# Kernel tuning notes

Hardware: AMD Instinct MI355X
Metric: run time of the kernel (lower is better)

The kernel has to match this reference:

```python
import jax, jax.numpy as jnp
import numpy as np

N_NODES = 100000
N_EDGES = 1600000
F_IN = 16
H = 64
N_LAYERS = 2
LN_EPS = 1e-5


def setup_inputs() -> dict:
    key = jax.random.key(0)
    ks = jax.random.split(key, 12)
    x = jax.random.normal(ks[0], (N_NODES, F_IN), dtype=jnp.float32)
    edge_index = jax.random.randint(ks[1], (2, N_EDGES), 0, N_NODES, dtype=jnp.int64)
    s = lambda fan_in: 1.0 / np.sqrt(fan_in)
    Wp = jax.random.uniform(ks[2], (H, F_IN), jnp.float32, -s(F_IN), s(F_IN))
    bp = jax.random.uniform(ks[3], (H,), jnp.float32, -s(F_IN), s(F_IN))
    # Per-layer SAGEConv params: lin_l (neighbor agg, with bias) and lin_r (root, no bias)
    Wl = jax.random.uniform(ks[4], (N_LAYERS, H, H), jnp.float32, -s(H), s(H))
    bl = jax.random.uniform(ks[5], (N_LAYERS, H), jnp.float32, -s(H), s(H))
    Wr = jax.random.uniform(ks[6], (N_LAYERS, H, H), jnp.float32, -s(H), s(H))
    gamma = jnp.ones((N_LAYERS, H), jnp.float32)
    beta = jnp.zeros((N_LAYERS, H), jnp.float32)
    W1 = jax.random.uniform(ks[7], (H // 2, H), jnp.float32, -s(H), s(H))
    b1 = jax.random.uniform(ks[8], (H // 2,), jnp.float32, -s(H), s(H))
    W2 = jax.random.uniform(ks[9], (1, H // 2), jnp.float32, -s(H // 2), s(H // 2))
    b2 = jax.random.uniform(ks[10], (1,), jnp.float32, -s(H // 2), s(H // 2))
    return {"x": x, "edge_index": edge_index, "Wp": Wp, "bp": bp, "Wl": Wl,
            "bl": bl, "Wr": Wr, "gamma": gamma, "beta": beta,
            "W1": W1, "b1": b1, "W2": W2, "b2": b2}


def _layernorm(h, g, b):
    mu = jnp.mean(h, axis=-1, keepdims=True)
    var = jnp.mean(jnp.square(h - mu), axis=-1, keepdims=True)
    return (h - mu) * jax.lax.rsqrt(var + LN_EPS) * g + b


def reference(x, edge_index, Wp, bp, Wl, bl, Wr, gamma, beta, W1, b1, W2, b2):
    N = x.shape[0]
    src, dst = edge_index[0], edge_index[1]
    # input projection + relu
    h = jax.nn.relu(x @ Wp.T + bp)  # [N, H]
    # in-degree for mean aggregation (empty-neighborhood mean -> 0, so clamp is safe
    # only because random graph; matches scatter_mean semantics via masked divide)
    deg = jax.ops.segment_sum(jnp.ones(src.shape, jnp.float32), dst, num_segments=N)
    inv_deg = jnp.where(deg > 0, 1.0 / jnp.maximum(deg, 1.0), 0.0)[:, None]  # [N,1]
    for i in range(Wl.shape[0]):
        identity = h
        agg = jax.ops.segment_sum(h[src], dst, num_segments=N) * inv_deg  # mean over neighbors
        out = agg @ Wl[i].T + bl[i] + h @ Wr[i].T  # SAGEConv
        out = _layernorm(out, gamma[i], beta[i])
        h = jax.nn.relu(out) + identity  # dropout inactive at eval
    h = jax.nn.relu(h @ W1.T + b1)
    y = h @ W2.T + b2  # [N, 1]
    return y.squeeze(-1)
```

## Files before the change

### kernel.cpp

```cpp
#include <hip/hip_runtime.h>
#include <hip/hip_fp16.h>

#define FIN 16
#define HH 64
#define BKT_SHIFT 9
#define BSZ (1 << BKT_SHIFT)
#define MAXBUCK 256
#define NBLK 128

static constexpr float LN_EPS = 1e-5f;

__device__ __forceinline__ float laneval(float v, int l) {
  return __uint_as_float(__builtin_amdgcn_readlane(__float_as_uint(v), l));
}
__device__ __forceinline__ int rfl(int v) { return __builtin_amdgcn_readfirstlane(v); }
__device__ __forceinline__ float rflf(float v) {
  return __uint_as_float(__builtin_amdgcn_readfirstlane(__float_as_uint(v)));
}

__global__ void k_detect(const unsigned int* ei, int E, int* flag) {
  int lane = threadIdx.x & 63;
  int n = (E < 64) ? E : 64;
  unsigned int hi = (lane < n) ? ei[2 * lane + 1] : 0u;
  unsigned long long nz = __ballot(hi != 0u);
  if (lane == 0) *flag = (nz == 0ull) ? 1 : 0;
}


__global__ __launch_bounds__(256) void k_bincount(const void* ei, int E,
                                                  const int* __restrict__ flag,
                                                  int* __restrict__ Cmat, int nbuck) {
  __shared__ int lh[MAXBUCK];
  const int is64 = *flag;
  int t = threadIdx.x, j = blockIdx.x;
  for (int b = t; b < nbuck; b += 256) lh[b] = 0;
  __syncthreads();
  int chunk = (E + gridDim.x - 1) / gridDim.x;
  int e0 = j * chunk, e1 = (e0 + chunk < E) ? (e0 + chunk) : E;
  for (int e = e0 + t; e < e1; e += 256) {
    int d = is64 ? (int)((const long long*)ei)[E + e] : ((const int*)ei)[E + e];
    atomicAdd(&lh[d >> BKT_SHIFT], 1);
  }
  __syncthreads();
  for (int b = t; b < nbuck; b += 256) Cmat[b * gridDim.x + j] = lh[b];
}

__global__ void k_scanC(int* __restrict__ C, int len) {
  __shared__ int sm[1024];
  __shared__ int carry;
  int t = threadIdx.x;
  if (t == 0) carry = 0;
  __syncthreads();
  for (int base = 0; base < len; base += 1024) {
    int i = base + t;
    int v = (i < len) ? C[i] : 0;
    sm[t] = v;
    __syncthreads();
    for (int off = 1; off < 1024; off <<= 1) {
      int x = (t >= off) ? sm[t - off] : 0;
      __syncthreads();
      sm[t] += x;
      __syncthreads();
    }
    if (i < len) C[i] = carry + sm[t] - v;
    __syncthreads();
    if (t == 0) carry += sm[1023];
    __syncthreads();
  }
}

__global__ __launch_bounds__(256) void k_binwrite(const void* ei, int E,
                                                  const int* __restrict__ flag,
                                                  const int* __restrict__ Cmat,
                                                  unsigned long long* __restrict__ ebuf,
                                                  int nbuck) {
  __shared__ int lcur[MAXBUCK];
  const int is64 = *flag;
  int t = threadIdx.x, j = blockIdx.x;
  for (int b = t; b < nbuck; b += 256) lcur[b] = Cmat[b * gridDim.x + j];
  __syncthreads();
  int chunk = (E + gridDim.x - 1) / gridDim.x;
  int e0 = j * chunk, e1 = (e0 + chunk < E) ? (e0 + chunk) : E;
  for (int e = e0 + t; e < e1; e += 256) {
    int s, d;
    if (is64) {
      const long long* p = (const long long*)ei;
      s = (int)p[e];
      d = (int)p[E + e];
    } else {
      const int* p = (const int*)ei;
      s = p[e];
      d = p[E + e];
    }
    int pos = atomicAdd(&lcur[d >> BKT_SHIFT], 1);
    ebuf[pos] = ((unsigned long long)(unsigned)d << 32) | (unsigned)s;
  }
}

__global__ __launch_bounds__(256) void k_binscatter(
    const unsigned long long* __restrict__ ebuf, const int* __restrict__ Cs,
    int E, int N, int nbuck, int* __restrict__ offsets,
    float* __restrict__ inv_deg, int* __restrict__ csr) {
  __shared__ int cnt[BSZ];
  __shared__ int sm[256];
  int b = blockIdx.x, t = threadIdx.x;
  int n0 = b << BKT_SHIFT;
  int nn = N - n0;
  if (nn > BSZ) nn = BSZ;
  int p0 = Cs[b * NBLK];
  int p1 = (b + 1 < nbuck) ? Cs[(b + 1) * NBLK] : E;

  for (int i = t; i < BSZ; i += 256) cnt[i] = 0;
  __syncthreads();
  for (int p = p0 + t; p < p1; p += 256) {
    int d = (int)(ebuf[p] >> 32);
    atomicAdd(&cnt[d - n0], 1);
  }
  __syncthreads();
  int c0 = cnt[2 * t], c1 = cnt[2 * t + 1];
  int ps = c0 + c1;
  sm[t] = ps;
  __syncthreads();
  for (int off = 1; off < 256; off <<= 1) {
    int x = (t >= off) ? sm[t - off] : 0;
    __syncthreads();
    sm[t] += x;
    __syncthreads();
  }
  int excl = sm[t] - ps;
  cnt[2 * t] = excl;
  cnt[2 * t + 1] = excl + c0;
  if (2 * t < nn) {
    offsets[n0 + 2 * t] = p0 + excl;
    inv_deg[n0 + 2 * t] = (c0 > 0) ? (1.0f / (float)c0) : 0.0f;
  }
  if (2 * t + 1 < nn) {
    offsets[n0 + 2 * t + 1] = p0 + excl + c0;
    inv_deg[n0 + 2 * t + 1] = (c1 > 0) ? (1.0f / (float)c1) : 0.0f;
  }
  if (b == nbuck - 1 && t == 0) offsets[N] = E;
  __syncthreads();
  for (int p = p0 + t; p < p1; p += 256) {
    unsigned long long pk = ebuf[p];
    int d = (int)(pk >> 32);
    int s = (int)(pk & 0xffffffffull);
    int pos = p0 + atomicAdd(&cnt[d - n0], 1);
    csr[pos] = s;
  }
}

__global__ __launch_bounds__(256) void k_inproj(const float* __restrict__ x,
                                                const float* __restrict__ Wp,
                                                const float* __restrict__ bp,
                                                float* __restrict__ h,
                                                __half* __restrict__ h16, int N) {
  int lane = threadIdx.x & 63;
  int wid = (blockIdx.x * blockDim.x + threadIdx.x) >> 6;
  int nwaves = (gridDim.x * blockDim.x) >> 6;
  float w[FIN];
#pragma unroll
  for (int k = 0; k < FIN; ++k) w[k] = Wp[lane * FIN + k];
  float b = bp[lane];
  for (int n = wid; n < N; n += nwaves) {
    const float4* xr = (const float4*)(x + (size_t)n * FIN);
    float a0 = b, a1 = 0.f;
#pragma unroll
    for (int q = 0; q < FIN / 4; ++q) {
      float4 xv = xr[q];
      a0 = fmaf(xv.x, w[4 * q + 0], a0);
      a1 = fmaf(xv.y, w[4 * q + 1], a1);
      a0 = fmaf(xv.z, w[4 * q + 2], a0);
      a1 = fmaf(xv.w, w[4 * q + 3], a1);
    }
    float r = fmaxf(a0 + a1, 0.0f);
    h[(size_t)n * HH + lane] = r;
    h16[(size_t)n * HH + lane] = __float2half(r);
  }
}

__global__ __launch_bounds__(256, 8) void k_gather(
    const __half* __restrict__ h16_in, const int* __restrict__ offsets,
    const int* __restrict__ csr, const float* __restrict__ inv_deg,
    __half* __restrict__ agg16, int N) {
  int lane = threadIdx.x & 63;
  int wid = (blockIdx.x * blockDim.x + threadIdx.x) >> 6;
  int nwaves = (gridDim.x * blockDim.x) >> 6;
  for (int n = wid; n < N; n += nwaves) {
    int p0 = rfl(offsets[n]);
    int p1 = rfl(offsets[n + 1]);
    float idg = rflf(inv_deg[n]);
    float a0 = 0.f, a1 = 0.f, a2 = 0.f, a3 = 0.f;
    int p = p0;
    for (; p + 16 <= p1; p += 16) {
      float v[16];
#pragma unroll
      for (int i = 0; i < 16; ++i) {
        int s = rfl(csr[p + i]);
        v[i] = __half2float(h16_in[(size_t)s * HH + lane]);
      }
      a0 += (v[0] + v[1]) + (v[2] + v[3]);
      a1 += (v[4] + v[5]) + (v[6] + v[7]);
      a2 += (v[8] + v[9]) + (v[10] + v[11]);
      a3 += (v[12] + v[13]) + (v[14] + v[15]);
    }
    for (; p + 4 <= p1; p += 4) {
      int s0 = rfl(csr[p + 0]), s1 = rfl(csr[p + 1]);
      int s2 = rfl(csr[p + 2]), s3 = rfl(csr[p + 3]);
      float v0 = __half2float(h16_in[(size_t)s0 * HH + lane]);
      float v1 = __half2float(h16_in[(size_t)s1 * HH + lane]);
      float v2 = __half2float(h16_in[(size_t)s2 * HH + lane]);
      float v3 = __half2float(h16_in[(size_t)s3 * HH + lane]);
      a0 += (v0 + v1) + (v2 + v3);
    }
    for (; p < p1; ++p) {
      int s = rfl(csr[p]);
      a0 += __half2float(h16_in[(size_t)s * HH + lane]);
    }
    agg16[(size_t)n * HH + lane] = __float2half(((a0 + a1) + (a2 + a3)) * idg);
  }
}

__global__ __launch_bounds__(256) void k_gemv(
    const float* __restrict__ h_in, const __half* __restrict__ agg16,
    float* __restrict__ h_out, __half* __restrict__ h16_out,
    const float* __restrict__ Wl, const float* __restrict__ bl,
    const float* __restrict__ Wr, const float* __restrict__ gamma,
    const float* __restrict__ beta, int N) {
  int lane = threadIdx.x & 63;
  int wid = (blockIdx.x * blockDim.x + threadIdx.x) >> 6;
  int nwaves = (gridDim.x * blockDim.x) >> 6;
  float blv = bl[lane], g = gamma[lane], be = beta[lane];
  const float4* wlr = (const float4*)(Wl + lane * HH);
  const float4* wrr = (const float4*)(Wr + lane * HH);

  for (int n = 2 * wid; n < N; n += 2 * nwaves) {
    int m2 = (n + 1 < N) ? (n + 1) : n;
    float hnA = h_in[(size_t)n * HH + lane];
    float hnB = h_in[(size_t)m2 * HH + lane];
    float acA = __half2float(agg16[(size_t)n * HH + lane]);
    float acB = __half2float(agg16[(size_t)m2 * HH + lane]);

    float olA = blv, orA = 0.f, olB = blv, orB = 0.f;
#pragma unroll
    for (int q = 0; q < HH / 4; ++q) {
      float4 wl4 = wlr[q];
      float4 wr4 = wrr[q];
      olA = fmaf(laneval(acA, 4 * q + 0), wl4.x, olA);
      olB = fmaf(laneval(acB, 4 * q + 0), wl4.x, olB);
      orA = fmaf(laneval(hnA, 4 * q + 0), wr4.x, orA);
      orB = fmaf(laneval(hnB, 4 * q + 0), wr4.x, orB);
      olA = fmaf(laneval(acA, 4 * q + 1), wl4.y, olA);
      olB = fmaf(laneval(acB, 4 * q + 1), wl4.y, olB);
      orA = fmaf(laneval(hnA, 4 * q + 1), wr4.y, orA);
      orB = fmaf(laneval(hnB, 4 * q + 1), wr4.y, orB);
      olA = fmaf(laneval(acA, 4 * q + 2), wl4.z, olA);
      olB = fmaf(laneval(acB, 4 * q + 2), wl4.z, olB);
      orA = fmaf(laneval(hnA, 4 * q + 2), wr4.z, orA);
      orB = fmaf(laneval(hnB, 4 * q + 2), wr4.z, orB);
      olA = fmaf(laneval(acA, 4 * q + 3), wl4.w, olA);
      olB = fmaf(laneval(acB, 4 * q + 3), wl4.w, olB);
      orA = fmaf(laneval(hnA, 4 * q + 3), wr4.w, orA);
      orB = fmaf(laneval(hnB, 4 * q + 3), wr4.w, orB);
    }

#pragma unroll
    for (int b = 0; b < 2; ++b) {
      float out = (b == 0) ? (olA + orA) : (olB + orB);
      float hn = (b == 0) ? hnA : hnB;
      int m = (b == 0) ? n : m2;
      float s = out;
#pragma unroll
      for (int msk = 1; msk < 64; msk <<= 1) s += __shfl_xor(s, msk);
      float mu = s * (1.0f / 64.0f);
      float d = out - mu;
      float vs = d * d;
#pragma unroll
      for (int msk = 1; msk < 64; msk <<= 1) vs += __shfl_xor(vs, msk);
      float var = vs * (1.0f / 64.0f);
      float val = fmaf(d * rsqrtf(var + LN_EPS), g, be);
      float res = fmaxf(val, 0.0f) + hn;
      h_out[(size_t)m * HH + lane] = res;
      h16_out[(size_t)m * HH + lane] = __float2half(res);
    }
  }
}

__global__ __launch_bounds__(256) void k_mlp(const float* __restrict__ h,
                                             const float* __restrict__ W1,
                                             const float* __restrict__ b1,
                                             const float* __restrict__ W2,
                                             const float* __restrict__ b2,
                                             float* __restrict__ y, int N) {
  int lane = threadIdx.x & 63;
  int half = lane >> 5;
  int j = lane & 31;
  int wid = (blockIdx.x * blockDim.x + threadIdx.x) >> 6;
  int nwaves = (gridDim.x * blockDim.x) >> 6;

  float w1[HH];
#pragma unroll
  for (int k = 0; k < HH; ++k) w1[k] = W1[j * HH + k];
  float b1v = b1[j], w2v = W2[j], b2v = b2[0];

  for (int base = wid * 2; base < N; base += nwaves * 2) {
    int n = base + half;
    float t0 = b1v, t1 = 0.0f;
    if (n < N) {
      const float4* hr = (const float4*)(h + (size_t)n * HH);
#pragma unroll
      for (int q = 0; q < HH / 4; ++q) {
        float4 hv = hr[q];
        t0 = fmaf(hv.x, w1[4 * q + 0], t0);
        t1 = fmaf(hv.y, w1[4 * q + 1], t1);
        t0 = fmaf(hv.z, w1[4 * q + 2], t0);
        t1 = fmaf(hv.w, w1[4 * q + 3], t1);
      }
    }
    float t = fmaxf(t0 + t1, 0.0f) * w2v;
#pragma unroll
    for (int m = 1; m < 32; m <<= 1) t += __shfl_xor(t, m);
    if (j == 0 && n < N) y[n] = t + b2v;
  }
}

extern "C" void kernel_launch(void* const* d_in, const int* in_sizes, int n_in,
                              void* d_out, int out_size, void* d_ws, size_t ws_size,
                              hipStream_t stream) {
  const float* x = (const float*)d_in[0];
  const void* ei = d_in[1];
  const float* Wp = (const float*)d_in[2];
  const float* bp = (const float*)d_in[3];
  const float* Wl = (const float*)d_in[4];
  const float* bl = (const float*)d_in[5];
  const float* Wr = (const float*)d_in[6];
  const float* gamma = (const float*)d_in[7];
  const float* beta = (const float*)d_in[8];
  const float* W1 = (const float*)d_in[9];
  const float* b1 = (const float*)d_in[10];
  const float* W2 = (const float*)d_in[11];
  const float* b2 = (const float*)d_in[12];
  float* y = (float*)d_out;

  const int N = in_sizes[0] / FIN;
  const int E = in_sizes[1] / 2;
  const int nbuck = (N + BSZ - 1) >> BKT_SHIFT;

  char* w = (char*)d_ws;
  auto carve = [&](size_t bytes) -> char* {
    char* p = w;
    w += (bytes + 255) / 256 * 256;
    return p;
  };
  int* offsets = (int*)carve(((size_t)N + 1) * 4);
  int* flag = (int*)carve(4);
  float* invdeg = (float*)carve((size_t)N * 4);
  int* csr = (int*)carve((size_t)E * 4);
  int* Cmat = (int*)carve((size_t)MAXBUCK * NBLK * 4);
  unsigned long long* ebuf = (unsigned long long*)carve((size_t)E * 8);
  float* hA = (float*)carve((size_t)N * HH * 4);
  float* hB = (float*)carve((size_t)N * HH * 4);
  __half* h16A = (__half*)carve((size_t)N * HH * 2);
  __half* h16B = (__half*)carve((size_t)N * HH * 2);
  __half* agg16 = (__half*)carve((size_t)N * HH * 2);

  k_detect<<<1, 64, 0, stream>>>((const unsigned int*)ei, E, flag);
  k_bincount<<<NBLK, 256, 0, stream>>>(ei, E, flag, Cmat, nbuck);
  k_scanC<<<1, 1024, 0, stream>>>(Cmat, nbuck * NBLK);
  k_binwrite<<<NBLK, 256, 0, stream>>>(ei, E, flag, Cmat, ebuf, nbuck);
  k_binscatter<<<nbuck, 256, 0, stream>>>(ebuf, Cmat, E, N, nbuck,
                                          offsets, invdeg, csr);
  k_inproj<<<1024, 256, 0, stream>>>(x, Wp, bp, hA, h16A, N);
  k_gather<<<2048, 256, 0, stream>>>(h16A, offsets, csr, invdeg, agg16, N);
  k_gemv<<<2048, 256, 0, stream>>>(hA, agg16, hB, h16B,
                                   Wl, bl, Wr, gamma, beta, N);
  k_gather<<<2048, 256, 0, stream>>>(h16B, offsets, csr, invdeg, agg16, N);
  k_gemv<<<2048, 256, 0, stream>>>(hB, agg16, hA, h16A,
                                   Wl + HH * HH, bl + HH, Wr + HH * HH,
                                   gamma + HH, beta + HH, N);
  k_mlp<<<512, 256, 0, stream>>>(hA, W1, b1, W2, b2, y, N);
}
```

Baseline: 450.5 us.

## Replace readlane GEMV in SAGE layers with fp16 MFMA 16x16x16 tiles

The per-node readlane/FMA GEMV for the SAGEConv linear layers is replaced by an MFMA kernel that handles 16 nodes per wave, using fp16 copies of the aggregated and root features. A small kernel converts Wl and Wr to fp16 once per call. LayerNorm is computed through 16-lane shuffles over the MFMA output layout. Using fp16 for h and the weights in the matmul lowers precision, and the output writes are now strided by column groups.

Result: faster. 398.2 us (-11.6%).

```diff
diff --git a/kernel.cpp b/kernel.cpp
--- a/kernel.cpp
+++ b/kernel.cpp
@@ -10,9 +10,9 @@
 
 static constexpr float LN_EPS = 1e-5f;
 
-__device__ __forceinline__ float laneval(float v, int l) {
-  return __uint_as_float(__builtin_amdgcn_readlane(__float_as_uint(v), l));
-}
+typedef _Float16 half4v __attribute__((ext_vector_type(4)));
+typedef float f32x4 __attribute__((ext_vector_type(4)));
+
 __device__ __forceinline__ int rfl(int v) { return __builtin_amdgcn_readfirstlane(v); }
 __device__ __forceinline__ float rflf(float v) {
   return __uint_as_float(__builtin_amdgcn_readfirstlane(__float_as_uint(v)));
@@ -24,6 +24,16 @@
   unsigned int hi = (lane < n) ? ei[2 * lane + 1] : 0u;
   unsigned long long nz = __ballot(hi != 0u);
   if (lane == 0) *flag = (nz == 0ull) ? 1 : 0;
+}
+
+__global__ void k_wconv(const float* __restrict__ Wl, const float* __restrict__ Wr,
+                        __half* __restrict__ Wl16, __half* __restrict__ Wr16,
+                        int count) {
+  int i = blockIdx.x * blockDim.x + threadIdx.x;
+  if (i < count) {
+    Wl16[i] = __float2half(Wl[i]);
+    Wr16[i] = __float2half(Wr[i]);
+  }
 }
 
 
@@ -220,67 +230,89 @@
   }
 }
 
-__global__ __launch_bounds__(256) void k_gemv(
-    const float* __restrict__ h_in, const __half* __restrict__ agg16,
+__global__ __launch_bounds__(256) void k_gemv_mfma(
+    const float* __restrict__ h_in, const __half* __restrict__ h16_in,
+    const __half* __restrict__ agg16,
     float* __restrict__ h_out, __half* __restrict__ h16_out,
-    const float* __restrict__ Wl, const float* __restrict__ bl,
-    const float* __restrict__ Wr, const float* __restrict__ gamma,
+    const __half* __restrict__ Wl16, const float* __restrict__ bl,
+    const __half* __restrict__ Wr16, const float* __restrict__ gamma,
     const float* __restrict__ beta, int N) {
   int lane = threadIdx.x & 63;
   int wid = (blockIdx.x * blockDim.x + threadIdx.x) >> 6;
   int nwaves = (gridDim.x * blockDim.x) >> 6;
-  float blv = bl[lane], g = gamma[lane], be = beta[lane];
-  const float4* wlr = (const float4*)(Wl + lane * HH);
-  const float4* wrr = (const float4*)(Wr + lane * HH);
-
-  for (int n = 2 * wid; n < N; n += 2 * nwaves) {
-    int m2 = (n + 1 < N) ? (n + 1) : n;
-    float hnA = h_in[(size_t)n * HH + lane];
-    float hnB = h_in[(size_t)m2 * HH + lane];
-    float acA = __half2float(agg16[(size_t)n * HH + lane]);
-    float acB = __half2float(agg16[(size_t)m2 * HH + lane]);
-
-    float olA = blv, orA = 0.f, olB = blv, orB = 0.f;
-#pragma unroll
-    for (int q = 0; q < HH / 4; ++q) {
-      float4 wl4 = wlr[q];
-      float4 wr4 = wrr[q];
-      olA = fmaf(laneval(acA, 4 * q + 0), wl4.x, olA);
-      olB = fmaf(laneval(acB, 4 * q + 0), wl4.x, olB);
-      orA = fmaf(laneval(hnA, 4 * q + 0), wr4.x, orA);
-      orB = fmaf(laneval(hnB, 4 * q + 0), wr4.x, orB);
-      olA = fmaf(laneval(acA, 4 * q + 1), wl4.y, olA);
-      olB = fmaf(laneval(acB, 4 * q + 1), wl4.y, olB);
-      orA = fmaf(laneval(hnA, 4 * q + 1), wr4.y, orA);
-      orB = fmaf(laneval(hnB, 4 * q + 1), wr4.y, orB);
-      olA = fmaf(laneval(acA, 4 * q + 2), wl4.z, olA);
-      olB = fmaf(laneval(acB, 4 * q + 2), wl4.z, olB);
-      orA = fmaf(laneval(hnA, 4 * q + 2), wr4.z, orA);
-      orB = fmaf(laneval(hnB, 4 * q + 2), wr4.z, orB);
-      olA = fmaf(laneval(acA, 4 * q + 3), wl4.w, olA);
-      olB = fmaf(laneval(acB, 4 * q + 3), wl4.w, olB);
-      orA = fmaf(laneval(hnA, 4 * q + 3), wr4.w, orA);
-      orB = fmaf(laneval(hnB, 4 * q + 3), wr4.w, orB);
-    }
-
-#pragma unroll
-    for (int b = 0; b < 2; ++b) {
-      float out = (b == 0) ? (olA + orA) : (olB + orB);
-      float hn = (b == 0) ? hnA : hnB;
-      int m = (b == 0) ? n : m2;
-      float s = out;
-#pragma unroll
-      for (int msk = 1; msk < 64; msk <<= 1) s += __shfl_xor(s, msk);
-      float mu = s * (1.0f / 64.0f);
-      float d = out - mu;
-      float vs = d * d;
-#pragma unroll
-      for (int msk = 1; msk < 64; msk <<= 1) vs += __shfl_xor(vs, msk);
-      float var = vs * (1.0f / 64.0f);
-      float val = fmaf(d * rsqrtf(var + LN_EPS), g, be);
-      float res = fmaxf(val, 0.0f) + hn;
-      h_out[(size_t)m * HH + lane] = res;
-      h16_out[(size_t)m * HH + lane] = __float2half(res);
+  int c = lane & 15;
+  int g = lane >> 4;
+
+  float bj[4], gm[4], bt[4];
+#pragma unroll
+  for (int u = 0; u < 4; ++u) {
+    bj[u] = bl[16 * u + c];
+    gm[u] = gamma[16 * u + c];
+    bt[u] = beta[16 * u + c];
+  }
+
+  int ntiles = (N + 15) >> 4;
+  for (int tile = wid; tile < ntiles; tile += nwaves) {
+    int n0 = tile << 4;
+    int rowA = n0 + c;
+    if (rowA > N - 1) rowA = N - 1;
+    const __half* arow = agg16 + (size_t)rowA * HH + 4 * g;
+    const __half* hrow = h16_in + (size_t)rowA * HH + 4 * g;
+
+    half4v aA[4], aH[4];
+#pragma unroll
+    for (int t = 0; t < 4; ++t) {
+      aA[t] = *(const half4v*)(arow + 16 * t);
+      aH[t] = *(const half4v*)(hrow + 16 * t);
+    }
+
+    f32x4 acc[4];
+#pragma unroll
+    for (int u = 0; u < 4; ++u) {
+      acc[u] = (f32x4){bj[u], bj[u], bj[u], bj[u]};
+#pragma unroll
+      for (int t = 0; t < 4; ++t) {
+        half4v bL = *(const half4v*)(Wl16 + (size_t)(16 * u + c) * HH + 16 * t + 4 * g);
+        half4v bR = *(const half4v*)(Wr16 + (size_t)(16 * u + c) * HH + 16 * t + 4 * g);
+        acc[u] = __builtin_amdgcn_mfma_f32_16x16x16f16(aA[t], bL, acc[u], 0, 0, 0);
+        acc[u] = __builtin_amdgcn_mfma_f32_16x16x16f16(aH[t], bR, acc[u], 0, 0, 0);
+      }
+    }
+
+    float mu[4], rs[4];
+#pragma unroll
+    for (int r = 0; r < 4; ++r) {
+      float s = (acc[0][r] + acc[1][r]) + (acc[2][r] + acc[3][r]);
+#pragma unroll
+      for (int m = 1; m < 16; m <<= 1) s += __shfl_xor(s, m);
+      mu[r] = s * (1.0f / 64.0f);
+    }
+#pragma unroll
+    for (int r = 0; r < 4; ++r) {
+      float v = 0.f;
+#pragma unroll
+      for (int u = 0; u < 4; ++u) {
+        float d = acc[u][r] - mu[r];
+        v += d * d;
+      }
+#pragma unroll
+      for (int m = 1; m < 16; m <<= 1) v += __shfl_xor(v, m);
+      rs[r] = rsqrtf(v * (1.0f / 64.0f) + LN_EPS);
+    }
+
+#pragma unroll
+    for (int u = 0; u < 4; ++u) {
+#pragma unroll
+      for (int r = 0; r < 4; ++r) {
+        int node = n0 + 4 * g + r;
+        int nl = (node < N) ? node : N - 1;
+        float val = fmaf((acc[u][r] - mu[r]) * rs[r], gm[u], bt[u]);
+        float res = fmaxf(val, 0.0f) + h_in[(size_t)nl * HH + 16 * u + c];
+        if (node < N) {
+          h_out[(size_t)node * HH + 16 * u + c] = res;
+          h16_out[(size_t)node * HH + 16 * u + c] = __float2half(res);
+        }
+      }
     }
   }
 }
@@ -362,8 +394,11 @@
   __half* h16A = (__half*)carve((size_t)N * HH * 2);
   __half* h16B = (__half*)carve((size_t)N * HH * 2);
   __half* agg16 = (__half*)carve((size_t)N * HH * 2);
+  __half* Wl16 = (__half*)carve((size_t)2 * HH * HH * 2);
+  __half* Wr16 = (__half*)carve((size_t)2 * HH * HH * 2);
 
   k_detect<<<1, 64, 0, stream>>>((const unsigned int*)ei, E, flag);
+  k_wconv<<<32, 256, 0, stream>>>(Wl, Wr, Wl16, Wr16, 2 * HH * HH);
   k_bincount<<<NBLK, 256, 0, stream>>>(ei, E, flag, Cmat, nbuck);
   k_scanC<<<1, 1024, 0, stream>>>(Cmat, nbuck * NBLK);
   k_binwrite<<<NBLK, 256, 0, stream>>>(ei, E, flag, Cmat, ebuf, nbuck);
@@ -371,11 +406,11 @@
                                           offsets, invdeg, csr);
   k_inproj<<<1024, 256, 0, stream>>>(x, Wp, bp, hA, h16A, N);
   k_gather<<<2048, 256, 0, stream>>>(h16A, offsets, csr, invdeg, agg16, N);
-  k_gemv<<<2048, 256, 0, stream>>>(hA, agg16, hB, h16B,
-                                   Wl, bl, Wr, gamma, beta, N);
+  k_gemv_mfma<<<1024, 256, 0, stream>>>(hA, h16A, agg16, hB, h16B,
+                                        Wl16, bl, Wr16, gamma, beta, N);
   k_gather<<<2048, 256, 0, stream>>>(h16B, offsets, csr, invdeg, agg16, N);
-  k_gemv<<<2048, 256, 0, stream>>>(hB, agg16, hA, h16A,
-                                   Wl + HH * HH, bl + HH, Wr + HH * HH,
-                                   gamma + HH, beta + HH, N);
+  k_gemv_mfma<<<1024, 256, 0, stream>>>(hB, h16B, agg16, hA, h16A,
+                                        Wl16 + HH * HH, bl + HH, Wr16 + HH * HH,
+                                        gamma + HH, beta + HH, N);
   k_mlp<<<512, 256, 0, stream>>>(hA, W1, b1, W2, b2, y, N);
 }
```
